# Kernel tuning notes

Measured on AMD Instinct MI355X. Metric: run time of the kernel, lower is better.

The kernel has to match this reference:

```python
import jax, jax.numpy as jnp
import numpy as np

B, H, W, C = 8, 256, 256, 96
WS, SHIFT, HEADS = 8, 4, 3
HD = C // HEADS
MLPD = 4 * C
EPS = 1e-5


def _rel_pos_index(ws):
    coords = np.stack(np.meshgrid(np.arange(ws), np.arange(ws), indexing='ij'))
    flat = coords.reshape(2, -1)
    rel = (flat[:, :, None] - flat[:, None, :]).transpose(1, 2, 0).copy()
    rel[:, :, 0] += ws - 1
    rel[:, :, 1] += ws - 1
    rel[:, :, 0] *= 2 * ws - 1
    return rel.sum(-1)  # (ws*ws, ws*ws) int


def _shift_attn_mask(h, w, ws, shift):
    # standard Swin shifted-window additive mask, shape (num_windows, N, N)
    img = np.zeros((h, w))
    cnt = 0
    for hs in (slice(0, -ws), slice(-ws, -shift), slice(-shift, None)):
        for wsl in (slice(0, -ws), slice(-ws, -shift), slice(-shift, None)):
            img[hs, wsl] = cnt
            cnt += 1
    mw = img.reshape(h // ws, ws, w // ws, ws).transpose(0, 2, 1, 3).reshape(-1, ws * ws)
    diff = mw[:, None, :] - mw[:, :, None]
    return np.where(diff != 0, -100.0, 0.0).astype(np.float32)


def _ln(x, g, b):
    mu = jnp.mean(x, -1, keepdims=True)
    var = jnp.mean(jnp.square(x - mu), -1, keepdims=True)
    return (x - mu) * jax.lax.rsqrt(var + EPS) * g + b


def setup_inputs() -> dict:
    key = jax.random.key(0)
    ks = jax.random.split(key, 12)
    w = lambda k, shape: (jax.random.normal(k, shape, jnp.float32) * 0.02)
    return {
        'hidden_states': jax.random.normal(ks[0], (B, H * W, C), jnp.float32),
        'ln1_g': jnp.ones((C,), jnp.float32), 'ln1_b': jnp.zeros((C,), jnp.float32),
        'Wq': w(ks[1], (C, C)), 'bq': jnp.zeros((C,), jnp.float32),
        'Wk': w(ks[2], (C, C)), 'bk': jnp.zeros((C,), jnp.float32),
        'Wv': w(ks[3], (C, C)), 'bv': jnp.zeros((C,), jnp.float32),
        'rel_bias_table': w(ks[4], ((2 * WS - 1) ** 2, HEADS)),
        'Wo': w(ks[5], (C, C)), 'bo': jnp.zeros((C,), jnp.float32),
        'ln2_g': jnp.ones((C,), jnp.float32), 'ln2_b': jnp.zeros((C,), jnp.float32),
        'W1': w(ks[6], (C, MLPD)), 'b1': jnp.zeros((MLPD,), jnp.float32),
        'W2': w(ks[7], (MLPD, C)), 'b2': jnp.zeros((C,), jnp.float32),
        'height': H, 'width': W,
    }


def reference(hidden_states, ln1_g, ln1_b, Wq, bq, Wk, bk, Wv, bv, rel_bias_table,
              Wo, bo, ln2_g, ln2_b, W1, b1, W2, b2, height, width):
    b, L, c = hidden_states.shape
    N = WS * WS
    shortcut = hidden_states
    x = _ln(hidden_states, ln1_g, ln1_b).reshape(b, height, width, c)
    # cyclic shift
    x = jnp.roll(x, (-SHIFT, -SHIFT), axis=(1, 2))
    nh, nw = height // WS, width // WS
    # window partition -> (b*nh*nw, N, c)
    xw = x.reshape(b, nh, WS, nw, WS, c).transpose(0, 1, 3, 2, 4, 5).reshape(-1, N, c)
    q = (xw @ Wq + bq).reshape(-1, N, HEADS, HD).transpose(0, 2, 1, 3)
    k = (xw @ Wk + bk).reshape(-1, N, HEADS, HD).transpose(0, 2, 1, 3)
    v = (xw @ Wv + bv).reshape(-1, N, HEADS, HD).transpose(0, 2, 1, 3)
    scores = jnp.einsum('whqd,whkd->whqk', q, k) / np.float32(np.sqrt(HD))
    rpi = jnp.asarray(_rel_pos_index(WS).reshape(-1))
    bias = rel_bias_table[rpi].reshape(N, N, HEADS).transpose(2, 0, 1)  # (heads, N, N)
    scores = scores + bias[None]
    mask = jnp.asarray(_shift_attn_mask(height, width, WS, SHIFT))  # (nWin, N, N)
    nWin = nh * nw
    scores = scores.reshape(b, nWin, HEADS, N, N) + mask[None, :, None]
    probs = jax.nn.softmax(scores.reshape(-1, HEADS, N, N), axis=-1)
    ctx = jnp.einsum('whqk,whkd->whqd', probs, v).transpose(0, 2, 1, 3).reshape(-1, N, c)
    attn_out = ctx @ Wo + bo
    # window reverse + reverse cyclic shift
    x = attn_out.reshape(b, nh, nw, WS, WS, c).transpose(0, 1, 3, 2, 4, 5).reshape(b, height, width, c)
    x = jnp.roll(x, (SHIFT, SHIFT), axis=(1, 2)).reshape(b, L, c)
    hidden = shortcut + x
    y = _ln(hidden, ln2_g, ln2_b)
    y = jax.nn.gelu(y @ W1 + b1, approximate=False)
    return hidden + y @ W2 + b2
```

## Files before the change

### kernel.cpp

```cpp
#include <hip/hip_runtime.h>
#include <hip/hip_bf16.h>
#include <stdint.h>

#define Bn      8
#define Hdim    256
#define Wdim    256
#define Cdim    96
#define WSZ     8
#define NSHIFT  4
#define NHEADS  3
#define HDim    32
#define Ntok    64
#define MLPDim  384

typedef __attribute__((ext_vector_type(8))) short short8b;
typedef __attribute__((ext_vector_type(4))) float f32x4;

#define WS_BIASB 221184
#define WS_TOTAL 284544
#define FB_QKV 0
#define FB_BO  1152
#define FB_B1  1536
#define FB_B2  3072
#define FB_L1G 3168
#define FB_L1B 3264
#define FB_L2G 3360
#define FB_L2B 3456
#define FB_BT  3552
#define FB_CNT 15840
__device__ __align__(16) unsigned char g_wsbuf[WS_TOTAL];

template <typename T> __device__ __forceinline__ float ldf(const T v);
template <> __device__ __forceinline__ float ldf<float>(const float v) { return v; }
template <> __device__ __forceinline__ float ldf<__hip_bfloat16>(const __hip_bfloat16 v) { return __bfloat162float(v); }

__device__ __forceinline__ int region(int p) {
    return p >= (Hdim - NSHIFT) ? 2 : (p >= (Hdim - WSZ) ? 1 : 0);
}

template <typename T>
__device__ __forceinline__ bool wrong_dtype(const T* ln1g) {
    const uint32_t tag = *reinterpret_cast<const uint32_t*>(ln1g);
    const uint32_t want = (sizeof(T) == 2) ? 0x3F803F80u : 0x3F800000u;
    return tag != want;
}

__device__ __forceinline__ uint32_t pk2(float a, float b) {
    union { __hip_bfloat162 h; uint32_t u; } c;
    c.h.x = __float2bfloat16(a);
    c.h.y = __float2bfloat16(b);
    return c.u;
}
__device__ __forceinline__ unsigned short bfu(float f) {
    union { __hip_bfloat16 b; unsigned short u; } c; c.b = __float2bfloat16(f); return c.u;
}

template <typename T>
__device__ __forceinline__ void load8f(const T* p, float* d) {
    if constexpr (sizeof(T) == 4) {
        const float4 a = *(const float4*)(p);
        const float4 b = *(const float4*)(p + 4);
        d[0]=a.x; d[1]=a.y; d[2]=a.z; d[3]=a.w; d[4]=b.x; d[5]=b.y; d[6]=b.z; d[7]=b.w;
    } else {
        union { uint4 u; unsigned short s[8]; } c; c.u = *(const uint4*)(p);
        #pragma unroll
        for (int j = 0; j < 8; j++) {
            union { unsigned short s; __hip_bfloat16 b; } t; t.s = c.s[j];
            d[j] = __bfloat162float(t.b);
        }
    }
}

__device__ __forceinline__ void wb() { __builtin_amdgcn_wave_barrier(); }

template <typename T>
__global__ __launch_bounds__(256) void swin_prep(
    const T* __restrict__ ln1g, const T* __restrict__ ln1b,
    const T* __restrict__ Wq, const T* __restrict__ bq,
    const T* __restrict__ Wk, const T* __restrict__ bk,
    const T* __restrict__ Wv, const T* __restrict__ bv,
    const T* __restrict__ btab,
    const T* __restrict__ Wo, const T* __restrict__ bo,
    const T* __restrict__ ln2g, const T* __restrict__ ln2b,
    const T* __restrict__ W1, const T* __restrict__ b1,
    const T* __restrict__ W2, const T* __restrict__ b2)
{
    if (wrong_dtype<T>(ln1g)) return;
    __hip_bfloat16* wbp = reinterpret_cast<__hip_bfloat16*>(g_wsbuf);
    float* fbp = reinterpret_cast<float*>(g_wsbuf + WS_BIASB);
    const int total = 110592 + FB_CNT;
    for (int idx = blockIdx.x * 256 + threadIdx.x; idx < total; idx += gridDim.x * 256) {
        if (idx < 110592) {
            const int f = idx >> 9, e = idx & 511;
            const int ln = e >> 3, j = e & 7, lr2 = ln & 15, lg2 = ln >> 4;
            float v;
            if (f < 54) {
                const int nt = f / 3, kt = f - 3 * nt;
                const int m = nt / 6, n = (nt - 6 * m) * 16 + lr2, k = 32 * kt + 8 * lg2 + j;
                const T* src = (m == 0) ? Wq : (m == 1) ? Wk : Wv;
                v = ldf<T>(src[k * 96 + n]);
            } else if (f < 72) {
                const int g = f - 54, nt = g / 3, kt = g - 3 * nt;
                v = ldf<T>(Wo[(32 * kt + 8 * lg2 + j) * 96 + 16 * nt + lr2]);
            } else if (f < 144) {
                const int g = f - 72, nt = g / 3, kt = g - 3 * nt;
                v = ldf<T>(W1[(32 * kt + 8 * lg2 + j) * 384 + 16 * nt + lr2]);
            } else {
                const int g = f - 144, nt = g / 12, kt = g - 12 * nt;
                v = ldf<T>(W2[(32 * kt + 8 * lg2 + j) * 96 + 16 * nt + lr2]);
            }
            wbp[idx] = __float2bfloat16(v);
        } else {
            const int i2 = idx - 110592;
            float v;
            if (i2 < FB_BO) {
                const int nt = i2 >> 6, ln = i2 & 63;
                const int m = nt / 6, n = (nt - 6 * m) * 16 + (ln & 15);
                v = ldf<T>((m == 0) ? bq[n] : (m == 1) ? bk[n] : bv[n]);
            } else if (i2 < FB_B1) {
                const int g = i2 - FB_BO, ln = g & 63;
                v = ldf<T>(bo[16 * (g >> 6) + (ln & 15)]);
            } else if (i2 < FB_B2) {
                const int g = i2 - FB_B1, ln = g & 63;
                v = ldf<T>(b1[16 * (g >> 6) + (ln & 15)]);
            } else if (i2 < FB_L1G) v = ldf<T>(b2[i2 - FB_B2]);
            else if (i2 < FB_L1B) v = ldf<T>(ln1g[i2 - FB_L1G]);
            else if (i2 < FB_L2G) v = ldf<T>(ln1b[i2 - FB_L1B]);
            else if (i2 < FB_L2B) v = ldf<T>(ln2g[i2 - FB_L2G]);
            else if (i2 < FB_BT)  v = ldf<T>(ln2b[i2 - FB_L2B]);
            else {
                const int e = i2 - FB_BT;
                const int r = e & 3, ln = (e >> 2) & 63, rest = e >> 8;
                const int mt2 = rest & 3, nt2 = (rest >> 2) & 3, hh = rest >> 4;
                const int q = 16 * mt2 + (ln & 15), k = 16 * nt2 + 4 * (ln >> 4) + r;
                const int qi = q >> 3, qj = q & 7, ki = k >> 3, kj = k & 7;
                v = ldf<T>(btab[((qi - ki + 7) * 15 + (qj - kj + 7)) * NHEADS + hh]);
            }
            fbp[i2] = v;
        }
    }
}

template <typename T>
__global__ __launch_bounds__(256, 4) void swin_mfma(
    const T* __restrict__ xin, const T* __restrict__ ln1g, T* __restrict__ out)
{
    if (wrong_dtype<T>(ln1g)) return;

    const short8b* WF = reinterpret_cast<const short8b*>(g_wsbuf);
    const float* fb = reinterpret_cast<const float*>(g_wsbuf + WS_BIASB);
    __shared__ __align__(16) char smem[36864];

    const int tid = threadIdx.x;
    const int wave = tid >> 6, lane = tid & 63;
    const int lg = lane >> 4, lr = lane & 15, mt = wave;
    const int tA = 16 * mt + lr;
    const int blk = blockIdx.x;
    const int b = blk >> 10, win = blk & 1023;
    const int wh = win >> 5, ww = win & 31;
    const int hq0 = wh * WSZ, wq0 = ww * WSZ;
    const uint32_t swzR  = (uint32_t)((lr & 7) << 4);
    const uint32_t slabA = (uint32_t)(mt * 3072);
    const uint32_t slabH = (uint32_t)(12288 + mt * 6144);

    const int iA = tA >> 3, jA = tA & 7;
    const int hA2 = (hq0 + iA + NSHIFT) & (Hdim - 1);
    const int wA2 = (wq0 + jA + NSHIFT) & (Wdim - 1);
    const size_t rowIdx = ((size_t)((b * Hdim + hA2) * Wdim + wA2)) * Cdim;
    const T* xrowA = xin + rowIdx;

    short8b xa[3];
    {
        float xv[24]; float s1 = 0.f, s2 = 0.f;
        #pragma unroll
        for (int kt = 0; kt < 3; kt++) {
            load8f<T>(xrowA + 32 * kt + 8 * lg, &xv[8 * kt]);
            #pragma unroll
            for (int j = 0; j < 8; j++) { s1 += xv[8*kt+j]; s2 += xv[8*kt+j] * xv[8*kt+j]; }
        }
        s1 += __shfl_xor(s1, 16); s2 += __shfl_xor(s2, 16);
        s1 += __shfl_xor(s1, 32); s2 += __shfl_xor(s2, 32);
        const float mu = s1 * (1.f / Cdim);
        const float rs = rsqrtf(s2 * (1.f / Cdim) - mu * mu + 1e-5f);
        #pragma unroll
        for (int kt = 0; kt < 3; kt++) {
            union { short8b v; unsigned short u[8]; } c;
            #pragma unroll
            for (int j = 0; j < 8; j++) {
                const int ch = 32 * kt + 8 * lg + j;
                c.u[j] = bfu((xv[8*kt+j] - mu) * rs * fb[FB_L1G + ch] + fb[FB_L1B + ch]);
            }
            xa[kt] = c.v;
        }
    }

    #pragma unroll 2
    for (int nt = 0; nt < 6; nt++) {
        f32x4 acc = {0.f, 0.f, 0.f, 0.f};
        #pragma unroll
        for (int kt = 0; kt < 3; kt++)
            acc = __builtin_amdgcn_mfma_f32_16x16x32_bf16(xa[kt], WF[(nt*3+kt)*64 + lane], acc, 0, 0, 0);
        const float bias = fb[FB_QKV + nt * 64 + lane];
        #pragma unroll
        for (int r = 0; r < 4; r++) {
            const int tl = 4 * lg + r;
            *(__hip_bfloat16*)(smem + ((slabA + tl * 192 + (16*nt+lr) * 2) ^ ((tl & 7) << 4))) =
                __float2bfloat16(acc[r] + bias);
        }
    }
    #pragma unroll 2
    for (int nt = 0; nt < 6; nt++) {
        f32x4 acc = {0.f, 0.f, 0.f, 0.f};
        #pragma unroll
        for (int kt = 0; kt < 3; kt++)
            acc = __builtin_amdgcn_mfma_f32_16x16x32_bf16(xa[kt], WF[((6+nt)*3+kt)*64 + lane], acc, 0, 0, 0);
        const float bias = fb[FB_QKV + (6 + nt) * 64 + lane];
        #pragma unroll
        for (int r = 0; r < 4; r++) {
            const int tok = 16 * mt + 4 * lg + r;
            *(__hip_bfloat16*)(smem + ((12288u + tok * 192 + (16*nt+lr) * 2) ^ ((tok & 7) << 4))) =
                __float2bfloat16(acc[r] + bias);
        }
    }
    #pragma unroll 2
    for (int nt = 0; nt < 6; nt++) {
        f32x4 acc = {0.f, 0.f, 0.f, 0.f};
        #pragma unroll
        for (int kt = 0; kt < 3; kt++)
            acc = __builtin_amdgcn_mfma_f32_16x16x32_bf16(xa[kt], WF[((12+nt)*3+kt)*64 + lane], acc, 0, 0, 0);
        const float bias = fb[FB_QKV + (12 + nt) * 64 + lane];
        const int d = 16 * nt + lr;
        #pragma unroll
        for (int r = 0; r < 4; r++)
            *(__hip_bfloat16*)(smem + ((24576u + d * 128 + (16*mt + 4*lg + r) * 2) ^ swzR)) =
                __float2bfloat16(acc[r] + bias);
    }
    __syncthreads();

    short8b qf[3];
    #pragma unroll
    for (int h2 = 0; h2 < 3; h2++)
        qf[h2] = *(const short8b*)(smem + ((slabA + lr * 192 + 64 * h2 + 16 * lg) ^ swzR));
    wb();

    const int qi = tA >> 3, qj = tA & 7;
    const int lq = region(hq0 + qi) * 3 + region(wq0 + qj);
    float mval[16];
    #pragma unroll
    for (int nt = 0; nt < 4; nt++)
        #pragma unroll
        for (int r = 0; r < 4; r++) {
            const int k = 16 * nt + 4 * lg + r;
            const int lk = region(hq0 + (k >> 3)) * 3 + region(wq0 + (k & 7));
            mval[4*nt+r] = (lq != lk) ? -100.f : 0.f;
        }

    f32x4 ctxr[3][2];
    #pragma unroll
    for (int h2 = 0; h2 < 3; h2++)
        #pragma unroll
        for (int dt = 0; dt < 2; dt++) ctxr[h2][dt] = (f32x4){0.f, 0.f, 0.f, 0.f};

    #pragma unroll
    for (int hh = 0; hh < NHEADS; hh++) {
        f32x4 sc[4];
        #pragma unroll
        for (int nt = 0; nt < 4; nt++) {
            const short8b kf = *(const short8b*)(smem + ((12288u + (16*nt+lr) * 192 + 64*hh + 16*lg) ^ swzR));
            f32x4 z = {0.f, 0.f, 0.f, 0.f};
            sc[nt] = __builtin_amdgcn_mfma_f32_16x16x32_bf16(kf, qf[hh], z, 0, 0, 0);
        }
        float p[16]; float mx = -1e30f;
        #pragma unroll
        for (int nt = 0; nt < 4; nt++) {
            const f32x4 bt = *(const f32x4*)(fb + FB_BT + ((hh * 4 + nt) * 4 + mt) * 256 + lane * 4);
            #pragma unroll
            for (int r = 0; r < 4; r++) {
                const float v = sc[nt][r] * 0.17677669529663687f + bt[r] + mval[4*nt+r];
                p[4*nt+r] = v; mx = fmaxf(mx, v);
            }
        }
        mx = fmaxf(mx, __shfl_xor(mx, 16)); mx = fmaxf(mx, __shfl_xor(mx, 32));
        float sum = 0.f;
        #pragma unroll
        for (int i = 0; i < 16; i++) { p[i] = __expf(p[i] - mx); sum += p[i]; }
        sum += __shfl_xor(sum, 16); sum += __shfl_xor(sum, 32);
        const float inv = 1.f / sum;
        #pragma unroll
        for (int nt = 0; nt < 4; nt++) {
            const uint32_t d0 = pk2(p[4*nt] * inv, p[4*nt+1] * inv);
            const uint32_t d1 = pk2(p[4*nt+2] * inv, p[4*nt+3] * inv);
            *(uint2*)(smem + ((slabA + lr * 128 + (16*nt + 4*lg) * 2) ^ swzR)) = make_uint2(d0, d1);
        }
        wb();
        short8b pb[2];
        #pragma unroll
        for (int kc = 0; kc < 2; kc++)
            pb[kc] = *(const short8b*)(smem + ((slabA + lr * 128 + 64 * kc + 16 * lg) ^ swzR));
        #pragma unroll
        for (int dt = 0; dt < 2; dt++) {
            const int drow = 32 * hh + 16 * dt + lr;
            #pragma unroll
            for (int kc = 0; kc < 2; kc++) {
                const short8b vf = *(const short8b*)(smem + ((24576u + drow * 128 + 64 * kc + 16 * lg) ^ swzR));
                ctxr[hh][dt] = __builtin_amdgcn_mfma_f32_16x16x32_bf16(vf, pb[kc], ctxr[hh][dt], 0, 0, 0);
            }
        }
        wb();
    }

    #pragma unroll
    for (int h2 = 0; h2 < 3; h2++)
        #pragma unroll
        for (int dt = 0; dt < 2; dt++) {
            const uint32_t d0 = pk2(ctxr[h2][dt][0], ctxr[h2][dt][1]);
            const uint32_t d1 = pk2(ctxr[h2][dt][2], ctxr[h2][dt][3]);
            const int ch = 32 * h2 + 16 * dt + 4 * lg;
            *(uint2*)(smem + ((slabA + lr * 192 + ch * 2) ^ swzR)) = make_uint2(d0, d1);
        }
    wb();
    short8b cA[3];
    #pragma unroll
    for (int kt = 0; kt < 3; kt++)
        cA[kt] = *(const short8b*)(smem + ((slabA + lr * 192 + 64 * kt + 16 * lg) ^ swzR));

    float hidc[6][4];
    #pragma unroll 2
    for (int nt = 0; nt < 6; nt++) {
        f32x4 acc = {0.f, 0.f, 0.f, 0.f};
        #pragma unroll
        for (int kt = 0; kt < 3; kt++)
            acc = __builtin_amdgcn_mfma_f32_16x16x32_bf16(cA[kt], WF[(54 + nt*3 + kt)*64 + lane], acc, 0, 0, 0);
        const float bias = fb[FB_BO + nt * 64 + lane];
        #pragma unroll
        for (int r = 0; r < 4; r++) hidc[nt][r] = acc[r] + bias;
    }
    __syncthreads();

    #pragma unroll
    for (int nt = 0; nt < 6; nt++)
        #pragma unroll
        for (int r = 0; r < 4; r++) {
            const int tl = 4 * lg + r;
            *(float*)(smem + ((slabH + tl * 384 + (16*nt+lr) * 4) ^ ((tl & 7) << 4))) = hidc[nt][r];
        }
    wb();
    float hidr[24];
    #pragma unroll
    for (int kt = 0; kt < 3; kt++) {
        const f32x4 h0 = *(const f32x4*)(smem + ((slabH + lr * 384 + 128 * kt + 32 * lg) ^ swzR));
        const f32x4 h1 = *(const f32x4*)(smem + ((slabH + lr * 384 + 128 * kt + 32 * lg + 16) ^ swzR));
        #pragma unroll
        for (int j = 0; j < 4; j++) { hidr[8*kt+j] = h0[j]; hidr[8*kt+4+j] = h1[j]; }
    }
    wb();
    #pragma unroll
    for (int kt = 0; kt < 3; kt++) {
        float t8[8]; load8f<T>(xrowA + 32 * kt + 8 * lg, t8);
        #pragma unroll
        for (int j = 0; j < 8; j++) hidr[8*kt+j] += t8[j];
    }
    short8b yA[3];
    {
        float s3 = 0.f, s4 = 0.f;
        #pragma unroll
        for (int i = 0; i < 24; i++) { s3 += hidr[i]; s4 += hidr[i] * hidr[i]; }
        s3 += __shfl_xor(s3, 16); s4 += __shfl_xor(s4, 16);
        s3 += __shfl_xor(s3, 32); s4 += __shfl_xor(s4, 32);
        const float mu = s3 * (1.f / Cdim);
        const float rs = rsqrtf(s4 * (1.f / Cdim) - mu * mu + 1e-5f);
        #pragma unroll
        for (int kt = 0; kt < 3; kt++) {
            union { short8b v; unsigned short u[8]; } c;
            #pragma unroll
            for (int j = 0; j < 8; j++) {
                const int ch = 32 * kt + 8 * lg + j;
                c.u[j] = bfu((hidr[8*kt+j] - mu) * rs * fb[FB_L2G + ch] + fb[FB_L2B + ch]);
            }
            yA[kt] = c.v;
        }
    }

    f32x4 acc2[6];
    #pragma unroll
    for (int nt = 0; nt < 6; nt++) acc2[nt] = (f32x4){0.f, 0.f, 0.f, 0.f};
    #pragma unroll
    for (int half = 0; half < 2; half++) {
        #pragma unroll 2
        for (int ntl = 0; ntl < 12; ntl++) {
            const int nt = 12 * half + ntl;
            f32x4 a1 = {0.f, 0.f, 0.f, 0.f};
            #pragma unroll
            for (int kt = 0; kt < 3; kt++)
                a1 = __builtin_amdgcn_mfma_f32_16x16x32_bf16(yA[kt], WF[(72 + nt*3 + kt)*64 + lane], a1, 0, 0, 0);
            const float bias = fb[FB_B1 + nt * 64 + lane];
            #pragma unroll
            for (int r = 0; r < 4; r++) {
                float u = a1[r] + bias;
                u = 0.5f * u * (1.f + erff(u * 0.70710678118654752f));
                const int tl = 4 * lg + r;
                *(__hip_bfloat16*)(smem + ((slabH + tl * 384 + (16*ntl+lr) * 2) ^ ((tl & 7) << 4))) =
                    __float2bfloat16(u);
            }
        }
        wb();
        #pragma unroll 2
        for (int ks = 0; ks < 6; ks++) {
            const short8b hA = *(const short8b*)(smem + ((slabH + lr * 384 + 64 * ks + 16 * lg) ^ swzR));
            #pragma unroll
            for (int nt = 0; nt < 6; nt++)
                acc2[nt] = __builtin_amdgcn_mfma_f32_16x16x32_bf16(
                    hA, WF[(144 + nt*12 + 6*half + ks)*64 + lane], acc2[nt], 0, 0, 0);
        }
        wb();
    }

    #pragma unroll
    for (int nt = 0; nt < 6; nt++)
        #pragma unroll
        for (int r = 0; r < 4; r++) {
            const int tl = 4 * lg + r;
            *(float*)(smem + ((slabH + tl * 384 + (16*nt+lr) * 4) ^ ((tl & 7) << 4))) = acc2[nt][r];
        }
    wb();
    T* outrow = out + rowIdx;
    #pragma unroll
    for (int kt = 0; kt < 3; kt++) {
        const f32x4 o0 = *(const f32x4*)(smem + ((slabH + lr * 384 + 128 * kt + 32 * lg) ^ swzR));
        const f32x4 o1 = *(const f32x4*)(smem + ((slabH + lr * 384 + 128 * kt + 32 * lg + 16) ^ swzR));
        float o[8];
        #pragma unroll
        for (int j = 0; j < 4; j++) {
            o[j]   = o0[j] + hidr[8*kt+j]   + fb[FB_B2 + 32*kt + 8*lg + j];
            o[4+j] = o1[j] + hidr[8*kt+4+j] + fb[FB_B2 + 32*kt + 8*lg + 4 + j];
        }
        if constexpr (sizeof(T) == 2) {
            uint4 u;
            u.x = pk2(o[0], o[1]); u.y = pk2(o[2], o[3]);
            u.z = pk2(o[4], o[5]); u.w = pk2(o[6], o[7]);
            *(uint4*)((__hip_bfloat16*)outrow + 32 * kt + 8 * lg) = u;
        } else {
            float4 f0 = {o[0], o[1], o[2], o[3]}, f1 = {o[4], o[5], o[6], o[7]};
            *(float4*)((float*)outrow + 32 * kt + 8 * lg) = f0;
            *(float4*)((float*)outrow + 32 * kt + 8 * lg + 4) = f1;
        }
    }
}

template <typename T>
static void launch_variant(void* const* d_in, void* d_out, hipStream_t stream) {
    swin_prep<T><<<494, 256, 0, stream>>>(
        (const T*)d_in[1],  (const T*)d_in[2],
        (const T*)d_in[3],  (const T*)d_in[4],
        (const T*)d_in[5],  (const T*)d_in[6],
        (const T*)d_in[7],  (const T*)d_in[8],
        (const T*)d_in[9],
        (const T*)d_in[10], (const T*)d_in[11],
        (const T*)d_in[12], (const T*)d_in[13],
        (const T*)d_in[14], (const T*)d_in[15],
        (const T*)d_in[16], (const T*)d_in[17]);
    swin_mfma<T><<<Bn * 1024, 256, 0, stream>>>(
        (const T*)d_in[0], (const T*)d_in[1], (T*)d_out);
}

extern "C" void kernel_launch(void* const* d_in, const int* in_sizes, int n_in,
                              void* d_out, int out_size, void* d_ws, size_t ws_size,
                              hipStream_t stream) {
    launch_variant<__hip_bfloat16>(d_in, d_out, stream);
    launch_variant<float>(d_in, d_out, stream);
}
```

Measured before the change: 758.4 us.

## Process two windows per block with two 16-row tiles per wave; use tanh-form GELU

Each 256-thread block now handles two adjacent windows. Each wave computes two 16-token M-tiles, so every weight fragment loaded from global memory feeds two MFMAs, which halves weight traffic per token. The grid is halved, shared memory doubles to 72KB and launch bounds drop to 2 blocks per SM. The exact erf GELU is replaced by a tanh/sigmoid approximation built on __expf, which cuts transcendental cost but adds a small numerical deviation.

```diff
diff --git a/kernel.cpp b/kernel.cpp
--- a/kernel.cpp
+++ b/kernel.cpp
@@ -53,6 +53,11 @@
 }
 __device__ __forceinline__ unsigned short bfu(float f) {
     union { __hip_bfloat16 b; unsigned short u; } c; c.b = __float2bfloat16(f); return c.u;
+}
+
+__device__ __forceinline__ float gelu_fast(float u) {
+    const float z = -1.5957691216057308f * u * (1.f + 0.044715f * u * u);
+    return u / (1.f + __expf(z));
 }
 
 template <typename T>
@@ -131,8 +136,8 @@
             else {
                 const int e = i2 - FB_BT;
                 const int r = e & 3, ln = (e >> 2) & 63, rest = e >> 8;
-                const int mt2 = rest & 3, nt2 = (rest >> 2) & 3, hh = rest >> 4;
-                const int q = 16 * mt2 + (ln & 15), k = 16 * nt2 + 4 * (ln >> 4) + r;
+                const int qt2 = rest & 3, nt2 = (rest >> 2) & 3, hh = rest >> 4;
+                const int q = 16 * qt2 + (ln & 15), k = 16 * nt2 + 4 * (ln >> 4) + r;
                 const int qi = q >> 3, qj = q & 7, ki = k >> 3, kj = k & 7;
                 v = ldf<T>(btab[((qi - ki + 7) * 15 + (qj - kj + 7)) * NHEADS + hh]);
             }
@@ -142,39 +147,46 @@
 }
 
 template <typename T>
-__global__ __launch_bounds__(256, 4) void swin_mfma(
+__global__ __launch_bounds__(256, 2) void swin_mfma(
     const T* __restrict__ xin, const T* __restrict__ ln1g, T* __restrict__ out)
 {
     if (wrong_dtype<T>(ln1g)) return;
 
     const short8b* WF = reinterpret_cast<const short8b*>(g_wsbuf);
     const float* fb = reinterpret_cast<const float*>(g_wsbuf + WS_BIASB);
-    __shared__ __align__(16) char smem[36864];
+    __shared__ __align__(16) char smem[73728];
 
     const int tid = threadIdx.x;
     const int wave = tid >> 6, lane = tid & 63;
-    const int lg = lane >> 4, lr = lane & 15, mt = wave;
-    const int tA = 16 * mt + lr;
+    const int lg = lane >> 4, lr = lane & 15;
+    const int half = wave & 1, wsel = wave >> 1;
     const int blk = blockIdx.x;
-    const int b = blk >> 10, win = blk & 1023;
-    const int wh = win >> 5, ww = win & 31;
+    const int b = blk >> 9, pw = blk & 511;
+    const int wh = pw >> 4, ww = ((pw & 15) << 1) | wsel;
     const int hq0 = wh * WSZ, wq0 = ww * WSZ;
-    const uint32_t swzR  = (uint32_t)((lr & 7) << 4);
-    const uint32_t slabA = (uint32_t)(mt * 3072);
-    const uint32_t slabH = (uint32_t)(12288 + mt * 6144);
-
-    const int iA = tA >> 3, jA = tA & 7;
-    const int hA2 = (hq0 + iA + NSHIFT) & (Hdim - 1);
-    const int wA2 = (wq0 + jA + NSHIFT) & (Wdim - 1);
-    const size_t rowIdx = ((size_t)((b * Hdim + hA2) * Wdim + wA2)) * Cdim;
-    const T* xrowA = xin + rowIdx;
-
-    short8b xa[3];
-    {
+    const uint32_t swzR = (uint32_t)((lr & 7) << 4);
+    const uint32_t AW = (uint32_t)(wave * 6144);
+    const uint32_t KW = 24576u + (uint32_t)wsel * 12288u;
+    const uint32_t VW = 49152u + (uint32_t)wsel * 12288u;
+    const uint32_t HW = 24576u + (uint32_t)wave * 12288u;
+
+    size_t rowIdx[2];
+    #pragma unroll
+    for (int mi = 0; mi < 2; mi++) {
+        const int t = 32 * half + 16 * mi + lr;
+        const int h2 = (hq0 + (t >> 3) + NSHIFT) & (Hdim - 1);
+        const int w2 = (wq0 + (t & 7) + NSHIFT) & (Wdim - 1);
+        rowIdx[mi] = ((size_t)((b * Hdim + h2) * Wdim + w2)) * Cdim;
+    }
+
+    short8b xa[2][3];
+    #pragma unroll
+    for (int mi = 0; mi < 2; mi++) {
+        const T* xrow = xin + rowIdx[mi];
         float xv[24]; float s1 = 0.f, s2 = 0.f;
         #pragma unroll
         for (int kt = 0; kt < 3; kt++) {
-            load8f<T>(xrowA + 32 * kt + 8 * lg, &xv[8 * kt]);
+            load8f<T>(xrow + 32 * kt + 8 * lg, &xv[8 * kt]);
             #pragma unroll
             for (int j = 0; j < 8; j++) { s1 += xv[8*kt+j]; s2 += xv[8*kt+j] * xv[8*kt+j]; }
         }
@@ -190,181 +202,225 @@
                 const int ch = 32 * kt + 8 * lg + j;
                 c.u[j] = bfu((xv[8*kt+j] - mu) * rs * fb[FB_L1G + ch] + fb[FB_L1B + ch]);
             }
-            xa[kt] = c.v;
+            xa[mi][kt] = c.v;
         }
     }
 
     #pragma unroll 2
     for (int nt = 0; nt < 6; nt++) {
-        f32x4 acc = {0.f, 0.f, 0.f, 0.f};
-        #pragma unroll
-        for (int kt = 0; kt < 3; kt++)
-            acc = __builtin_amdgcn_mfma_f32_16x16x32_bf16(xa[kt], WF[(nt*3+kt)*64 + lane], acc, 0, 0, 0);
+        f32x4 a0 = {0.f,0.f,0.f,0.f}, a1 = {0.f,0.f,0.f,0.f};
+        #pragma unroll
+        for (int kt = 0; kt < 3; kt++) {
+            const short8b bw = WF[(nt*3+kt)*64 + lane];
+            a0 = __builtin_amdgcn_mfma_f32_16x16x32_bf16(xa[0][kt], bw, a0, 0, 0, 0);
+            a1 = __builtin_amdgcn_mfma_f32_16x16x32_bf16(xa[1][kt], bw, a1, 0, 0, 0);
+        }
         const float bias = fb[FB_QKV + nt * 64 + lane];
         #pragma unroll
         for (int r = 0; r < 4; r++) {
-            const int tl = 4 * lg + r;
-            *(__hip_bfloat16*)(smem + ((slabA + tl * 192 + (16*nt+lr) * 2) ^ ((tl & 7) << 4))) =
-                __float2bfloat16(acc[r] + bias);
+            const int wl0 = 4 * lg + r;
+            const uint32_t sz = (uint32_t)((wl0 & 7) << 4);
+            *(__hip_bfloat16*)(smem + ((AW + wl0 * 192 + (16*nt+lr) * 2) ^ sz)) = __float2bfloat16(a0[r] + bias);
+            *(__hip_bfloat16*)(smem + ((AW + (wl0+16) * 192 + (16*nt+lr) * 2) ^ sz)) = __float2bfloat16(a1[r] + bias);
         }
     }
     #pragma unroll 2
     for (int nt = 0; nt < 6; nt++) {
-        f32x4 acc = {0.f, 0.f, 0.f, 0.f};
-        #pragma unroll
-        for (int kt = 0; kt < 3; kt++)
-            acc = __builtin_amdgcn_mfma_f32_16x16x32_bf16(xa[kt], WF[((6+nt)*3+kt)*64 + lane], acc, 0, 0, 0);
+        f32x4 a0 = {0.f,0.f,0.f,0.f}, a1 = {0.f,0.f,0.f,0.f};
+        #pragma unroll
+        for (int kt = 0; kt < 3; kt++) {
+            const short8b bw = WF[((6+nt)*3+kt)*64 + lane];
+            a0 = __builtin_amdgcn_mfma_f32_16x16x32_bf16(xa[0][kt], bw, a0, 0, 0, 0);
+            a1 = __builtin_amdgcn_mfma_f32_16x16x32_bf16(xa[1][kt], bw, a1, 0, 0, 0);
+        }
         const float bias = fb[FB_QKV + (6 + nt) * 64 + lane];
         #pragma unroll
         for (int r = 0; r < 4; r++) {
-            const int tok = 16 * mt + 4 * lg + r;
-            *(__hip_bfloat16*)(smem + ((12288u + tok * 192 + (16*nt+lr) * 2) ^ ((tok & 7) << 4))) =
-                __float2bfloat16(acc[r] + bias);
+            const int kt0 = 32 * half + 4 * lg + r;
+            const uint32_t sz = (uint32_t)((kt0 & 7) << 4);
+            *(__hip_bfloat16*)(smem + ((KW + kt0 * 192 + (16*nt+lr) * 2) ^ sz)) = __float2bfloat16(a0[r] + bias);
+            *(__hip_bfloat16*)(smem + ((KW + (kt0+16) * 192 + (16*nt+lr) * 2) ^ sz)) = __float2bfloat16(a1[r] + bias);
         }
     }
     #pragma unroll 2
     for (int nt = 0; nt < 6; nt++) {
-        f32x4 acc = {0.f, 0.f, 0.f, 0.f};
-        #pragma unroll
-        for (int kt = 0; kt < 3; kt++)
-            acc = __builtin_amdgcn_mfma_f32_16x16x32_bf16(xa[kt], WF[((12+nt)*3+kt)*64 + lane], acc, 0, 0, 0);
+        f32x4 a0 = {0.f,0.f,0.f,0.f}, a1 = {0.f,0.f,0.f,0.f};
+        #pragma unroll
+        for (int kt = 0; kt < 3; kt++) {
+            const short8b bw = WF[((12+nt)*3+kt)*64 + lane];
+            a0 = __builtin_amdgcn_mfma_f32_16x16x32_bf16(xa[0][kt], bw, a0, 0, 0, 0);
+            a1 = __builtin_amdgcn_mfma_f32_16x16x32_bf16(xa[1][kt], bw, a1, 0, 0, 0);
+        }
         const float bias = fb[FB_QKV + (12 + nt) * 64 + lane];
         const int d = 16 * nt + lr;
-        #pragma unroll
-        for (int r = 0; r < 4; r++)
-            *(__hip_bfloat16*)(smem + ((24576u + d * 128 + (16*mt + 4*lg + r) * 2) ^ swzR)) =
-                __float2bfloat16(acc[r] + bias);
+        const int tok0 = 32 * half + 4 * lg;
+        *(uint2*)(smem + ((VW + d * 128 + tok0 * 2) ^ swzR)) =
+            make_uint2(pk2(a0[0]+bias, a0[1]+bias), pk2(a0[2]+bias, a0[3]+bias));
+        *(uint2*)(smem + ((VW + d * 128 + (tok0+16) * 2) ^ swzR)) =
+            make_uint2(pk2(a1[0]+bias, a1[1]+bias), pk2(a1[2]+bias, a1[3]+bias));
     }
     __syncthreads();
 
-    short8b qf[3];
-    #pragma unroll
-    for (int h2 = 0; h2 < 3; h2++)
-        qf[h2] = *(const short8b*)(smem + ((slabA + lr * 192 + 64 * h2 + 16 * lg) ^ swzR));
+    short8b qf[2][3];
+    #pragma unroll
+    for (int mi = 0; mi < 2; mi++)
+        #pragma unroll
+        for (int hh = 0; hh < 3; hh++) {
+            const int wl = 16 * mi + lr;
+            qf[mi][hh] = *(const short8b*)(smem + ((AW + wl * 192 + (32*hh + 8*lg) * 2) ^ swzR));
+        }
     wb();
 
-    const int qi = tA >> 3, qj = tA & 7;
-    const int lq = region(hq0 + qi) * 3 + region(wq0 + qj);
-    float mval[16];
+    int lq[2];
+    #pragma unroll
+    for (int mi = 0; mi < 2; mi++) {
+        const int t = 32 * half + 16 * mi + lr;
+        lq[mi] = region(hq0 + (t >> 3)) * 3 + region(wq0 + (t & 7));
+    }
+    int lkv[16];
     #pragma unroll
     for (int nt = 0; nt < 4; nt++)
         #pragma unroll
         for (int r = 0; r < 4; r++) {
             const int k = 16 * nt + 4 * lg + r;
-            const int lk = region(hq0 + (k >> 3)) * 3 + region(wq0 + (k & 7));
-            mval[4*nt+r] = (lq != lk) ? -100.f : 0.f;
-        }
-
-    f32x4 ctxr[3][2];
-    #pragma unroll
-    for (int h2 = 0; h2 < 3; h2++)
-        #pragma unroll
-        for (int dt = 0; dt < 2; dt++) ctxr[h2][dt] = (f32x4){0.f, 0.f, 0.f, 0.f};
+            lkv[4*nt+r] = region(hq0 + (k >> 3)) * 3 + region(wq0 + (k & 7));
+        }
+
+    f32x4 ctxr[2][3][2];
+    #pragma unroll
+    for (int mi = 0; mi < 2; mi++)
+        #pragma unroll
+        for (int h2 = 0; h2 < 3; h2++)
+            #pragma unroll
+            for (int dt = 0; dt < 2; dt++) ctxr[mi][h2][dt] = (f32x4){0.f, 0.f, 0.f, 0.f};
 
     #pragma unroll
     for (int hh = 0; hh < NHEADS; hh++) {
-        f32x4 sc[4];
+        f32x4 sc[2][4];
         #pragma unroll
         for (int nt = 0; nt < 4; nt++) {
-            const short8b kf = *(const short8b*)(smem + ((12288u + (16*nt+lr) * 192 + 64*hh + 16*lg) ^ swzR));
+            const short8b kf = *(const short8b*)(smem + ((KW + (16*nt+lr) * 192 + (32*hh + 8*lg) * 2) ^ swzR));
             f32x4 z = {0.f, 0.f, 0.f, 0.f};
-            sc[nt] = __builtin_amdgcn_mfma_f32_16x16x32_bf16(kf, qf[hh], z, 0, 0, 0);
-        }
-        float p[16]; float mx = -1e30f;
-        #pragma unroll
-        for (int nt = 0; nt < 4; nt++) {
-            const f32x4 bt = *(const f32x4*)(fb + FB_BT + ((hh * 4 + nt) * 4 + mt) * 256 + lane * 4);
-            #pragma unroll
-            for (int r = 0; r < 4; r++) {
-                const float v = sc[nt][r] * 0.17677669529663687f + bt[r] + mval[4*nt+r];
-                p[4*nt+r] = v; mx = fmaxf(mx, v);
-            }
-        }
-        mx = fmaxf(mx, __shfl_xor(mx, 16)); mx = fmaxf(mx, __shfl_xor(mx, 32));
-        float sum = 0.f;
-        #pragma unroll
-        for (int i = 0; i < 16; i++) { p[i] = __expf(p[i] - mx); sum += p[i]; }
-        sum += __shfl_xor(sum, 16); sum += __shfl_xor(sum, 32);
-        const float inv = 1.f / sum;
-        #pragma unroll
-        for (int nt = 0; nt < 4; nt++) {
-            const uint32_t d0 = pk2(p[4*nt] * inv, p[4*nt+1] * inv);
-            const uint32_t d1 = pk2(p[4*nt+2] * inv, p[4*nt+3] * inv);
-            *(uint2*)(smem + ((slabA + lr * 128 + (16*nt + 4*lg) * 2) ^ swzR)) = make_uint2(d0, d1);
+            sc[0][nt] = __builtin_amdgcn_mfma_f32_16x16x32_bf16(kf, qf[0][hh], z, 0, 0, 0);
+            sc[1][nt] = __builtin_amdgcn_mfma_f32_16x16x32_bf16(kf, qf[1][hh], z, 0, 0, 0);
+        }
+        #pragma unroll
+        for (int mi = 0; mi < 2; mi++) {
+            const int qt = 2 * half + mi;
+            float p[16]; float mx = -1e30f;
+            #pragma unroll
+            for (int nt = 0; nt < 4; nt++) {
+                const f32x4 bt = *(const f32x4*)(fb + FB_BT + ((hh * 4 + nt) * 4 + qt) * 256 + lane * 4);
+                #pragma unroll
+                for (int r = 0; r < 4; r++) {
+                    float v = sc[mi][nt][r] * 0.17677669529663687f + bt[r];
+                    if (lq[mi] != lkv[4*nt+r]) v -= 100.f;
+                    p[4*nt+r] = v; mx = fmaxf(mx, v);
+                }
+            }
+            mx = fmaxf(mx, __shfl_xor(mx, 16)); mx = fmaxf(mx, __shfl_xor(mx, 32));
+            float sum = 0.f;
+            #pragma unroll
+            for (int i = 0; i < 16; i++) { p[i] = __expf(p[i] - mx); sum += p[i]; }
+            sum += __shfl_xor(sum, 16); sum += __shfl_xor(sum, 32);
+            const float inv = 1.f / sum;
+            #pragma unroll
+            for (int nt = 0; nt < 4; nt++) {
+                const uint32_t d0 = pk2(p[4*nt] * inv, p[4*nt+1] * inv);
+                const uint32_t d1 = pk2(p[4*nt+2] * inv, p[4*nt+3] * inv);
+                *(uint2*)(smem + ((AW + mi * 2048 + lr * 128 + (16*nt + 4*lg) * 2) ^ swzR)) = make_uint2(d0, d1);
+            }
         }
         wb();
-        short8b pb[2];
-        #pragma unroll
-        for (int kc = 0; kc < 2; kc++)
-            pb[kc] = *(const short8b*)(smem + ((slabA + lr * 128 + 64 * kc + 16 * lg) ^ swzR));
-        #pragma unroll
-        for (int dt = 0; dt < 2; dt++) {
-            const int drow = 32 * hh + 16 * dt + lr;
+        short8b pb[2][2];
+        #pragma unroll
+        for (int mi = 0; mi < 2; mi++)
+            #pragma unroll
+            for (int kc = 0; kc < 2; kc++)
+                pb[mi][kc] = *(const short8b*)(smem + ((AW + mi * 2048 + lr * 128 + (32*kc + 8*lg) * 2) ^ swzR));
+        #pragma unroll
+        for (int dt = 0; dt < 2; dt++)
             #pragma unroll
             for (int kc = 0; kc < 2; kc++) {
-                const short8b vf = *(const short8b*)(smem + ((24576u + drow * 128 + 64 * kc + 16 * lg) ^ swzR));
-                ctxr[hh][dt] = __builtin_amdgcn_mfma_f32_16x16x32_bf16(vf, pb[kc], ctxr[hh][dt], 0, 0, 0);
-            }
-        }
+                const short8b vf = *(const short8b*)(smem + ((VW + (32*hh + 16*dt + lr) * 128 + (32*kc + 8*lg) * 2) ^ swzR));
+                ctxr[0][hh][dt] = __builtin_amdgcn_mfma_f32_16x16x32_bf16(vf, pb[0][kc], ctxr[0][hh][dt], 0, 0, 0);
+                ctxr[1][hh][dt] = __builtin_amdgcn_mfma_f32_16x16x32_bf16(vf, pb[1][kc], ctxr[1][hh][dt], 0, 0, 0);
+            }
         wb();
     }
 
     #pragma unroll
-    for (int h2 = 0; h2 < 3; h2++)
-        #pragma unroll
-        for (int dt = 0; dt < 2; dt++) {
-            const uint32_t d0 = pk2(ctxr[h2][dt][0], ctxr[h2][dt][1]);
-            const uint32_t d1 = pk2(ctxr[h2][dt][2], ctxr[h2][dt][3]);
-            const int ch = 32 * h2 + 16 * dt + 4 * lg;
-            *(uint2*)(smem + ((slabA + lr * 192 + ch * 2) ^ swzR)) = make_uint2(d0, d1);
-        }
+    for (int mi = 0; mi < 2; mi++) {
+        const int wl = 16 * mi + lr;
+        #pragma unroll
+        for (int h2 = 0; h2 < 3; h2++)
+            #pragma unroll
+            for (int dt = 0; dt < 2; dt++) {
+                const uint32_t d0 = pk2(ctxr[mi][h2][dt][0], ctxr[mi][h2][dt][1]);
+                const uint32_t d1 = pk2(ctxr[mi][h2][dt][2], ctxr[mi][h2][dt][3]);
+                *(uint2*)(smem + ((AW + wl * 192 + (32*h2 + 16*dt + 4*lg) * 2) ^ swzR)) = make_uint2(d0, d1);
+            }
+    }
     wb();
-    short8b cA[3];
-    #pragma unroll
-    for (int kt = 0; kt < 3; kt++)
-        cA[kt] = *(const short8b*)(smem + ((slabA + lr * 192 + 64 * kt + 16 * lg) ^ swzR));
-
-    float hidc[6][4];
+    short8b cA[2][3];
+    #pragma unroll
+    for (int mi = 0; mi < 2; mi++)
+        #pragma unroll
+        for (int kt = 0; kt < 3; kt++)
+            cA[mi][kt] = *(const short8b*)(smem + ((AW + (16*mi+lr) * 192 + (32*kt + 8*lg) * 2) ^ swzR));
+
+    float hidc[2][6][4];
     #pragma unroll 2
     for (int nt = 0; nt < 6; nt++) {
-        f32x4 acc = {0.f, 0.f, 0.f, 0.f};
-        #pragma unroll
-        for (int kt = 0; kt < 3; kt++)
-            acc = __builtin_amdgcn_mfma_f32_16x16x32_bf16(cA[kt], WF[(54 + nt*3 + kt)*64 + lane], acc, 0, 0, 0);
+        f32x4 a0 = {0.f,0.f,0.f,0.f}, a1 = {0.f,0.f,0.f,0.f};
+        #pragma unroll
+        for (int kt = 0; kt < 3; kt++) {
+            const short8b bw = WF[(54 + nt*3 + kt)*64 + lane];
+            a0 = __builtin_amdgcn_mfma_f32_16x16x32_bf16(cA[0][kt], bw, a0, 0, 0, 0);
+            a1 = __builtin_amdgcn_mfma_f32_16x16x32_bf16(cA[1][kt], bw, a1, 0, 0, 0);
+        }
         const float bias = fb[FB_BO + nt * 64 + lane];
         #pragma unroll
-        for (int r = 0; r < 4; r++) hidc[nt][r] = acc[r] + bias;
+        for (int r = 0; r < 4; r++) { hidc[0][nt][r] = a0[r] + bias; hidc[1][nt][r] = a1[r] + bias; }
     }
     __syncthreads();
 
     #pragma unroll
-    for (int nt = 0; nt < 6; nt++)
-        #pragma unroll
-        for (int r = 0; r < 4; r++) {
-            const int tl = 4 * lg + r;
-            *(float*)(smem + ((slabH + tl * 384 + (16*nt+lr) * 4) ^ ((tl & 7) << 4))) = hidc[nt][r];
-        }
+    for (int mi = 0; mi < 2; mi++)
+        #pragma unroll
+        for (int nt = 0; nt < 6; nt++)
+            #pragma unroll
+            for (int r = 0; r < 4; r++) {
+                const int wl = 16 * mi + 4 * lg + r;
+                *(float*)(smem + ((HW + wl * 384 + (16*nt+lr) * 4) ^ ((wl & 7) << 4))) = hidc[mi][nt][r];
+            }
     wb();
-    float hidr[24];
-    #pragma unroll
-    for (int kt = 0; kt < 3; kt++) {
-        const f32x4 h0 = *(const f32x4*)(smem + ((slabH + lr * 384 + 128 * kt + 32 * lg) ^ swzR));
-        const f32x4 h1 = *(const f32x4*)(smem + ((slabH + lr * 384 + 128 * kt + 32 * lg + 16) ^ swzR));
-        #pragma unroll
-        for (int j = 0; j < 4; j++) { hidr[8*kt+j] = h0[j]; hidr[8*kt+4+j] = h1[j]; }
+    float hidr[2][24];
+    #pragma unroll
+    for (int mi = 0; mi < 2; mi++) {
+        const int wl = 16 * mi + lr;
+        #pragma unroll
+        for (int kt = 0; kt < 3; kt++) {
+            const f32x4 h0 = *(const f32x4*)(smem + ((HW + wl * 384 + (32*kt + 8*lg) * 4) ^ swzR));
+            const f32x4 h1 = *(const f32x4*)(smem + ((HW + wl * 384 + (32*kt + 8*lg) * 4 + 16) ^ swzR));
+            #pragma unroll
+            for (int j = 0; j < 4; j++) { hidr[mi][8*kt+j] = h0[j]; hidr[mi][8*kt+4+j] = h1[j]; }
+        }
     }
     wb();
-    #pragma unroll
-    for (int kt = 0; kt < 3; kt++) {
-        float t8[8]; load8f<T>(xrowA + 32 * kt + 8 * lg, t8);
-        #pragma unroll
-        for (int j = 0; j < 8; j++) hidr[8*kt+j] += t8[j];
-    }
-    short8b yA[3];
-    {
+    short8b yA[2][3];
+    #pragma unroll
+    for (int mi = 0; mi < 2; mi++) {
+        const T* xrow = xin + rowIdx[mi];
+        #pragma unroll
+        for (int kt = 0; kt < 3; kt++) {
+            float t8[8]; load8f<T>(xrow + 32 * kt + 8 * lg, t8);
+            #pragma unroll
+            for (int j = 0; j < 8; j++) hidr[mi][8*kt+j] += t8[j];
+        }
         float s3 = 0.f, s4 = 0.f;
         #pragma unroll
-        for (int i = 0; i < 24; i++) { s3 += hidr[i]; s4 += hidr[i] * hidr[i]; }
+        for (int i = 0; i < 24; i++) { s3 += hidr[mi][i]; s4 += hidr[mi][i] * hidr[mi][i]; }
         s3 += __shfl_xor(s3, 16); s4 += __shfl_xor(s4, 16);
         s3 += __shfl_xor(s3, 32); s4 += __shfl_xor(s4, 32);
         const float mu = s3 * (1.f / Cdim);
@@ -375,74 +431,87 @@
             #pragma unroll
             for (int j = 0; j < 8; j++) {
                 const int ch = 32 * kt + 8 * lg + j;
-                c.u[j] = bfu((hidr[8*kt+j] - mu) * rs * fb[FB_L2G + ch] + fb[FB_L2B + ch]);
-            }
-            yA[kt] = c.v;
-        }
-    }
-
-    f32x4 acc2[6];
-    #pragma unroll
-    for (int nt = 0; nt < 6; nt++) acc2[nt] = (f32x4){0.f, 0.f, 0.f, 0.f};
-    #pragma unroll
-    for (int half = 0; half < 2; half++) {
+                c.u[j] = bfu((hidr[mi][8*kt+j] - mu) * rs * fb[FB_L2G + ch] + fb[FB_L2B + ch]);
+            }
+            yA[mi][kt] = c.v;
+        }
+    }
+
+    f32x4 acc2[6][2];
+    #pragma unroll
+    for (int nt = 0; nt < 6; nt++) { acc2[nt][0] = (f32x4){0.f,0.f,0.f,0.f}; acc2[nt][1] = (f32x4){0.f,0.f,0.f,0.f}; }
+    #pragma unroll
+    for (int hf = 0; hf < 2; hf++) {
         #pragma unroll 2
         for (int ntl = 0; ntl < 12; ntl++) {
-            const int nt = 12 * half + ntl;
-            f32x4 a1 = {0.f, 0.f, 0.f, 0.f};
-            #pragma unroll
-            for (int kt = 0; kt < 3; kt++)
-                a1 = __builtin_amdgcn_mfma_f32_16x16x32_bf16(yA[kt], WF[(72 + nt*3 + kt)*64 + lane], a1, 0, 0, 0);
+            const int nt = 12 * hf + ntl;
+            f32x4 a0 = {0.f,0.f,0.f,0.f}, a1 = {0.f,0.f,0.f,0.f};
+            #pragma unroll
+            for (int kt = 0; kt < 3; kt++) {
+                const short8b bw = WF[(72 + nt*3 + kt)*64 + lane];
+                a0 = __builtin_amdgcn_mfma_f32_16x16x32_bf16(yA[0][kt], bw, a0, 0, 0, 0);
+                a1 = __builtin_amdgcn_mfma_f32_16x16x32_bf16(yA[1][kt], bw, a1, 0, 0, 0);
+            }
             const float bias = fb[FB_B1 + nt * 64 + lane];
             #pragma unroll
             for (int r = 0; r < 4; r++) {
-                float u = a1[r] + bias;
-                u = 0.5f * u * (1.f + erff(u * 0.70710678118654752f));
-                const int tl = 4 * lg + r;
-                *(__hip_bfloat16*)(smem + ((slabH + tl * 384 + (16*ntl+lr) * 2) ^ ((tl & 7) << 4))) =
-                    __float2bfloat16(u);
+                const float u0 = gelu_fast(a0[r] + bias);
+                const float u1 = gelu_fast(a1[r] + bias);
+                const int wl0 = 4 * lg + r;
+                const uint32_t sz = (uint32_t)((wl0 & 7) << 4);
+                *(__hip_bfloat16*)(smem + ((HW + wl0 * 384 + (16*ntl+lr) * 2) ^ sz)) = __float2bfloat16(u0);
+                *(__hip_bfloat16*)(smem + ((HW + (wl0+16) * 384 + (16*ntl+lr) * 2) ^ sz)) = __float2bfloat16(u1);
             }
         }
         wb();
         #pragma unroll 2
         for (int ks = 0; ks < 6; ks++) {
-            const short8b hA = *(const short8b*)(smem + ((slabH + lr * 384 + 64 * ks + 16 * lg) ^ swzR));
-            #pragma unroll
-            for (int nt = 0; nt < 6; nt++)
-                acc2[nt] = __builtin_amdgcn_mfma_f32_16x16x32_bf16(
-                    hA, WF[(144 + nt*12 + 6*half + ks)*64 + lane], acc2[nt], 0, 0, 0);
+            const short8b hA0 = *(const short8b*)(smem + ((HW + lr * 384 + 64*ks + 16*lg) ^ swzR));
+            const short8b hA1 = *(const short8b*)(smem + ((HW + (16+lr) * 384 + 64*ks + 16*lg) ^ swzR));
+            #pragma unroll
+            for (int nt = 0; nt < 6; nt++) {
+                const short8b bw = WF[(144 + nt*12 + 6*hf + ks)*64 + lane];
+                acc2[nt][0] = __builtin_amdgcn_mfma_f32_16x16x32_bf16(hA0, bw, acc2[nt][0], 0, 0, 0);
+                acc2[nt][1] = __builtin_amdgcn_mfma_f32_16x16x32_bf16(hA1, bw, acc2[nt][1], 0, 0, 0);
+            }
         }
         wb();
     }
 
     #pragma unroll
-    for (int nt = 0; nt < 6; nt++)
-        #pragma unroll
-        for (int r = 0; r < 4; r++) {
-            const int tl = 4 * lg + r;
-            *(float*)(smem + ((slabH + tl * 384 + (16*nt+lr) * 4) ^ ((tl & 7) << 4))) = acc2[nt][r];
-        }
+    for (int mi = 0; mi < 2; mi++)
+        #pragma unroll
+        for (int nt = 0; nt < 6; nt++)
+            #pragma unroll
+            for (int r = 0; r < 4; r++) {
+                const int wl = 16 * mi + 4 * lg + r;
+                *(float*)(smem + ((HW + wl * 384 + (16*nt+lr) * 4) ^ ((wl & 7) << 4))) = acc2[nt][mi][r];
+            }
     wb();
-    T* outrow = out + rowIdx;
-    #pragma unroll
-    for (int kt = 0; kt < 3; kt++) {
-        const f32x4 o0 = *(const f32x4*)(smem + ((slabH + lr * 384 + 128 * kt + 32 * lg) ^ swzR));
-        const f32x4 o1 = *(const f32x4*)(smem + ((slabH + lr * 384 + 128 * kt + 32 * lg + 16) ^ swzR));
-        float o[8];
-        #pragma unroll
-        for (int j = 0; j < 4; j++) {
-            o[j]   = o0[j] + hidr[8*kt+j]   + fb[FB_B2 + 32*kt + 8*lg + j];
-            o[4+j] = o1[j] + hidr[8*kt+4+j] + fb[FB_B2 + 32*kt + 8*lg + 4 + j];
-        }
-        if constexpr (sizeof(T) == 2) {
-            uint4 u;
-            u.x = pk2(o[0], o[1]); u.y = pk2(o[2], o[3]);
-            u.z = pk2(o[4], o[5]); u.w = pk2(o[6], o[7]);
-            *(uint4*)((__hip_bfloat16*)outrow + 32 * kt + 8 * lg) = u;
-        } else {
-            float4 f0 = {o[0], o[1], o[2], o[3]}, f1 = {o[4], o[5], o[6], o[7]};
-            *(float4*)((float*)outrow + 32 * kt + 8 * lg) = f0;
-            *(float4*)((float*)outrow + 32 * kt + 8 * lg + 4) = f1;
+    #pragma unroll
+    for (int mi = 0; mi < 2; mi++) {
+        T* outrow = out + rowIdx[mi];
+        const int wl = 16 * mi + lr;
+        #pragma unroll
+        for (int kt = 0; kt < 3; kt++) {
+            const f32x4 o0 = *(const f32x4*)(smem + ((HW + wl * 384 + (32*kt + 8*lg) * 4) ^ swzR));
+            const f32x4 o1 = *(const f32x4*)(smem + ((HW + wl * 384 + (32*kt + 8*lg) * 4 + 16) ^ swzR));
+            float o[8];
+            #pragma unroll
+            for (int j = 0; j < 4; j++) {
+                o[j]   = o0[j] + hidr[mi][8*kt+j]   + fb[FB_B2 + 32*kt + 8*lg + j];
+                o[4+j] = o1[j] + hidr[mi][8*kt+4+j] + fb[FB_B2 + 32*kt + 8*lg + 4 + j];
+            }
+            if constexpr (sizeof(T) == 2) {
+                uint4 u;
+                u.x = pk2(o[0], o[1]); u.y = pk2(o[2], o[3]);
+                u.z = pk2(o[4], o[5]); u.w = pk2(o[6], o[7]);
+                *(uint4*)((__hip_bfloat16*)outrow + 32 * kt + 8 * lg) = u;
+            } else {
+                float4 f0 = {o[0], o[1], o[2], o[3]}, f1 = {o[4], o[5], o[6], o[7]};
+                *(float4*)((float*)outrow + 32 * kt + 8 * lg) = f0;
+                *(float4*)((float*)outrow + 32 * kt + 8 * lg + 4) = f1;
+            }
         }
     }
 }
@@ -459,7 +528,7 @@
         (const T*)d_in[12], (const T*)d_in[13],
         (const T*)d_in[14], (const T*)d_in[15],
         (const T*)d_in[16], (const T*)d_in[17]);
-    swin_mfma<T><<<Bn * 1024, 256, 0, stream>>>(
+    swin_mfma<T><<<Bn * 512, 256, 0, stream>>>(
         (const T*)d_in[0], (const T*)d_in[1], (T*)d_out);
 }
 
```

New measurement: 771.1 us. No clear change (+1.7%).
